# Kernel optimization log

Measured on AMD Instinct MI355X. Metric: run time of the kernel, lower is better.

Reference implementation:

```python
import jax, jax.numpy as jnp
import numpy as np

STRIDES = [8, 16, 32, 64, 128]
FSIZES = [64, 32, 16, 8, 4]          # 512x512 input
NUM_CLASSES = 80
POS_THR, NEG_THR = 0.5, 0.4          # MaxIOUAssigner thresholds
BETA = 1.0 / 9.0                      # SmoothL1 beta (from loss_bbox cfg)
BBOX_W = 10.0                         # SmoothL1 loss_weight
ALPHA, GAMMA = 0.25, 2.0              # sigmoid focal loss


def _gen_anchors():
    """RetinaNet-style grid anchors, xyxy, concatenated over levels -> [A,4]."""
    ratios = np.array([0.5, 1.0, 2.0])
    scales = 4.0 * 2.0 ** (np.arange(3) / 3.0)   # octave_base_scale=4, 3 octaves
    levels = []
    for s, f in zip(STRIDES, FSIZES):
        ws = (s * scales[None, :] / np.sqrt(ratios)[:, None]).reshape(-1)  # [9]
        hs = (s * scales[None, :] * np.sqrt(ratios)[:, None]).reshape(-1)
        c = (np.arange(f) + 0.5) * s
        sx, sy = np.meshgrid(c, c)
        cxy = np.stack([sx, sy], -1).reshape(-1, 1, 2)   # [f*f,1,2]
        wh = np.stack([ws, hs], -1)[None]                # [1,9,2]
        a = np.concatenate([cxy - wh / 2, cxy + wh / 2], -1).reshape(-1, 4)
        levels.append(a)
    return jnp.asarray(np.concatenate(levels, 0), dtype=jnp.float32)  # [49104,4]


def _iou(anchors, gt):  # [A,4],[M,4] -> [A,M]
    area_a = (anchors[:, 2] - anchors[:, 0]) * (anchors[:, 3] - anchors[:, 1])
    area_g = (gt[:, 2] - gt[:, 0]) * (gt[:, 3] - gt[:, 1])
    lt = jnp.maximum(anchors[:, None, :2], gt[None, :, :2])
    rb = jnp.minimum(anchors[:, None, 2:], gt[None, :, 2:])
    wh = jnp.clip(rb - lt, 0.0)
    inter = wh[..., 0] * wh[..., 1]
    return inter / jnp.maximum(area_a[:, None] + area_g[None, :] - inter, 1e-6)


def _encode(boxes, anchors):  # DeltaXYWH encode, target_stds = 1
    aw = anchors[:, 2] - anchors[:, 0]
    ah = anchors[:, 3] - anchors[:, 1]
    ax = (anchors[:, 0] + anchors[:, 2]) * 0.5
    ay = (anchors[:, 1] + anchors[:, 3]) * 0.5
    gw = jnp.maximum(boxes[:, 2] - boxes[:, 0], 1e-6)
    gh = jnp.maximum(boxes[:, 3] - boxes[:, 1], 1e-6)
    gx = (boxes[:, 0] + boxes[:, 2]) * 0.5
    gy = (boxes[:, 1] + boxes[:, 3]) * 0.5
    return jnp.stack([(gx - ax) / aw, (gy - ay) / ah,
                      jnp.log(gw / aw), jnp.log(gh / ah)], -1)


def _assign_one(gt_boxes, gt_labels, gt_mask, anchors):
    """Per-image: IoU match, pseudo-sample, gather matched GT, encode, masks."""
    iou = _iou(anchors, gt_boxes)                      # [A,M]
    iou = jnp.where(gt_mask[None, :], iou, -1.0)       # kill padded GTs
    best = jnp.argmax(iou, 1)                          # [A]
    best_iou = jnp.max(iou, 1)
    # matched index: >=0 matched, -1 background, -2 ignored
    idx = jnp.where(best_iou >= POS_THR, best,
                    jnp.where(best_iou < NEG_THR, -1, -2))
    pos = idx >= 0
    matched = jnp.where(pos[:, None], gt_boxes[best], 0.0)   # gather_based_on_match
    reg_t = _encode(matched, anchors)
    total = jnp.maximum(1.0, jnp.sum(pos.astype(jnp.float32)))
    mask_reg = pos.astype(jnp.float32)[:, None] / total      # [A,1] -> broadcast 4
    labels = jnp.where(pos, gt_labels[best], -1)             # bg/ignored -> -1
    mask_cls = (idx >= -1).astype(jnp.float32) / total       # matched + background
    return reg_t, mask_reg, labels, mask_cls


def setup_inputs() -> dict:
    key = jax.random.key(0)
    ks = jax.random.split(key, 6)
    B, M, A, C = 16, 100, 49104, NUM_CLASSES
    cls_score = jax.random.normal(ks[0], (B, A, C), jnp.float32)
    bbox_pred = jax.random.normal(ks[1], (B, A, 4), jnp.float32) * 0.1
    cxy = jax.random.uniform(ks[2], (B, M, 2), jnp.float32, 50.0, 462.0)
    wh = jax.random.uniform(ks[3], (B, M, 2), jnp.float32, 16.0, 128.0)
    target_boxes = jnp.concatenate([cxy - wh / 2, cxy + wh / 2], -1)
    target_labels = jax.random.randint(ks[4], (B, M), 0, C, jnp.int32)
    mask_labels = jax.random.randint(ks[5], (B, M), 0, 2, jnp.int32).astype(bool)
    return {"cls_score": cls_score, "bbox_pred": bbox_pred,
            "target_boxes": target_boxes, "target_labels": target_labels,
            "mask_labels": mask_labels}


def reference(cls_score, bbox_pred, target_boxes, target_labels, mask_labels):
    anchors = _gen_anchors()                                        # [A,4]
    reg_t, mask_reg, labels, mask_cls = jax.vmap(
        _assign_one, in_axes=(0, 0, 0, None))(
        target_boxes, target_labels, mask_labels, anchors)          # per image
    bs = float(cls_score.shape[0])
    # SmoothL1 (beta=1/9, weight 10), masked + normalized per image
    d = jnp.abs(bbox_pred - reg_t)
    l1 = jnp.where(d < BETA, 0.5 * d * d / BETA, d - 0.5 * BETA)
    loss_bbox = BBOX_W * jnp.sum(l1 * mask_reg) / bs
    # sigmoid focal loss
    t = jax.nn.one_hot(labels, NUM_CLASSES, dtype=cls_score.dtype)  # -1 -> all-zero
    bce = t * jax.nn.softplus(-cls_score) + (1.0 - t) * jax.nn.softplus(cls_score)
    p = jax.nn.sigmoid(cls_score)
    pt = t * p + (1.0 - t) * (1.0 - p)
    at = ALPHA * t + (1.0 - ALPHA) * (1.0 - t)
    focal = at * (1.0 - pt) ** GAMMA * bce
    loss_cls = jnp.sum(focal * mask_cls[..., None]) / bs
    return jnp.stack([loss_cls, loss_bbox])
```

## Files before the change

### kernel.cpp

```cpp
#include <hip/hip_runtime.h>

#define N_ANCH 49104
#define NB_IMG 16
#define NGT 100
#define NC 80
#define BPIA 128
#define BPIB 192
#define NA_BLK (BPIA * NB_IMG)
#define NB_BLK (BPIB * NB_IMG)
#define IMG_F4 (N_ANCH * NC / 4)
#define OFF_C NA_BLK
#define OFF_B (NA_BLK + NB_BLK)
#define OFF_P (NA_BLK + 2 * NB_BLK)

#define LOG2E 1.4426950408889634f
#define LN2   0.6931471805599453f
#define FSCALE (0.75f * LN2)

__device__ __forceinline__ float frcp(float x){ return __builtin_amdgcn_rcpf(x); }
__device__ __forceinline__ float fexp2(float x){ return __builtin_amdgcn_exp2f(x); }
__device__ __forceinline__ float flog2(float x){ return __builtin_amdgcn_logf(x); }

__device__ __forceinline__ float f0_acc(float x, float acc){
  float xl = x * LOG2E;
  float mx = fmaxf(xl, 0.f);
  float mn = fminf(xl, 0.f);
  float u  = fexp2(mn - mx);
  float w  = 1.0f + u;
  float lw = flog2(w);
  float g  = mn - lw;
  float p2 = fexp2(g + g);
  return fmaf(p2, lw + mx, acc);
}

__device__ __forceinline__ float corr_term(float x){
  float xl = x * LOG2E;
  float mx = fmaxf(xl, 0.f);
  float mn = fminf(xl, 0.f);
  float u  = fexp2(mn - mx);
  float w  = 1.0f + u;
  float lw = flog2(w);
  float p2   = fexp2(2.f * (mn - lw));
  float omp2 = fexp2(-2.f * (mx + lw));
  float sp   = LN2 * (lw + mx);
  float spn  = LN2 * (lw - mn);
  return 0.25f * omp2 * spn - 0.75f * p2 * sp;
}

__global__ __launch_bounds__(256, 6) void fused_loss_kernel(
    const float* __restrict__ cls,
    const float* __restrict__ bbox,
    const float* __restrict__ gtb,
    const int*   __restrict__ gtl,
    const unsigned char* __restrict__ gmask,
    float* __restrict__ ws)
{
  const int tid = threadIdx.x;
  const int wv = tid >> 6, ln = tid & 63;

  __shared__ float  s_r0[4], s_r1[4], s_r2[4];
  __shared__ float  s_wmin[4], s_wmax[4];
  __shared__ float4 s_cgt[NGT + 4];
  __shared__ float  s_carea[NGT + 4];
  __shared__ int    s_clab[NGT + 4];
  __shared__ int    s_cnt;

  const int idx = blockIdx.x;
  const int role = idx % 5;

  if (role < 2){
    int aid = (idx / 5) * 2 + role;
    int b = aid / BPIA, s = aid % BPIA;
    const float4* p = (const float4*)cls + (size_t)b * IMG_F4;
    float a0 = 0.f, a1 = 0.f, a2 = 0.f, a3 = 0.f;
    #pragma unroll 2
    for (int i = s * 256 + tid; i < IMG_F4; i += BPIA * 256){
      float4 c4 = p[i];
      a0 = f0_acc(c4.x, a0); a1 = f0_acc(c4.y, a1);
      a2 = f0_acc(c4.z, a2); a3 = f0_acc(c4.w, a3);
    }
    float acc = (a0 + a1) + (a2 + a3);
    #pragma unroll
    for (int o = 32; o > 0; o >>= 1) acc += __shfl_down(acc, o);
    if (ln == 0) s_r0[wv] = acc;
    __syncthreads();
    if (tid == 0) ws[aid] = s_r0[0] + s_r0[1] + s_r0[2] + s_r0[3];
    return;
  }

  int bid = (idx / 5) * 3 + (role - 2);
  int b = bid / BPIB, blkc = bid % BPIB;
  int a = blkc * 256 + tid;
  bool va = a < N_ANCH;

  float x1, y1, x2, y2, areaA;
  if (va){
    int f, lg, st, rel;
    if      (a < 36864){ f = 64; lg = 6; st = 8;   rel = a; }
    else if (a < 46080){ f = 32; lg = 5; st = 16;  rel = a - 36864; }
    else if (a < 48384){ f = 16; lg = 4; st = 32;  rel = a - 46080; }
    else if (a < 48960){ f = 8;  lg = 3; st = 64;  rel = a - 48384; }
    else               { f = 4;  lg = 2; st = 128; rel = a - 48960; }
    int cell = rel / 9;
    int k    = rel - cell * 9;
    int yy   = cell >> lg;
    int xx   = cell & (f - 1);
    int rr = (k >= 6) ? 2 : ((k >= 3) ? 1 : 0);
    int sc = k - rr * 3;
    double sq  = (rr == 0) ? 0.7071067811865476 : ((rr == 1) ? 1.0 : 1.4142135623730951);
    double scl = (sc == 0) ? 4.0 : ((sc == 1) ? 5.039684199579493 : 6.349604207872798);
    double ss  = (double)st * scl;
    double wd  = ss / sq, hd = ss * sq;
    double cxd = ((double)xx + 0.5) * (double)st;
    double cyd = ((double)yy + 0.5) * (double)st;
    x1 = (float)(cxd - wd * 0.5);
    y1 = (float)(cyd - hd * 0.5);
    x2 = (float)(cxd + wd * 0.5);
    y2 = (float)(cyd + hd * 0.5);
    areaA = (x2 - x1) * (y2 - y1);
  } else { x1 = 0.f; y1 = 3.0e38f; x2 = 0.f; y2 = -3.0e38f; areaA = 1.f; }

  {
    float wy1 = y1, wy2 = y2;
    #pragma unroll
    for (int o = 32; o > 0; o >>= 1){
      wy1 = fminf(wy1, __shfl_down(wy1, o));
      wy2 = fmaxf(wy2, __shfl_down(wy2, o));
    }
    if (ln == 0){ s_wmin[wv] = wy1; s_wmax[wv] = wy2; }
  }
  __syncthreads();

  if (wv == 0){
    const unsigned int* mw = (const unsigned int*)gmask;
    bool nf = false, ob = false;
    for (int i = ln; i < (NB_IMG * NGT) / 4; i += 64){
      unsigned int w = mw[i];
      nf |= (w != 0u && w != 0x3F800000u);
      ob |= ((w & 0xFFFFFF00u) != 0u);
    }
    bool byteLayout = __any((int)nf) && __any((int)ob);
    float ymin = fminf(fminf(s_wmin[0], s_wmin[1]), fminf(s_wmin[2], s_wmin[3]));
    float ymax = fmaxf(fmaxf(s_wmax[0], s_wmax[1]), fmaxf(s_wmax[2], s_wmax[3]));
    const float4* g4 = (const float4*)gtb;

    float4 g = g4[b * NGT + ln];
    int v = byteLayout ? (gmask[b * NGT + ln] != 0)
                       : (((const unsigned int*)gmask)[b * NGT + ln] != 0u);
    bool pass = v && (g.y < ymax) && (g.w > ymin);
    unsigned long long bal = __ballot(pass);
    int pre = __popcll(bal & ((1ull << ln) - 1ull));
    if (pass){
      s_cgt[pre] = g;
      s_carea[pre] = (g.z - g.x) * (g.w - g.y);
      s_clab[pre] = gtl[b * NGT + ln];
    }
    int c0 = __popcll(bal);
    bool pass1 = false; float4 g1;
    if (ln < NGT - 64){
      g1 = g4[b * NGT + 64 + ln];
      int v1 = byteLayout ? (gmask[b * NGT + 64 + ln] != 0)
                          : (((const unsigned int*)gmask)[b * NGT + 64 + ln] != 0u);
      pass1 = v1 && (g1.y < ymax) && (g1.w > ymin);
    }
    unsigned long long bal1 = __ballot(pass1);
    int pre1 = c0 + __popcll(bal1 & ((1ull << ln) - 1ull));
    if (pass1){
      s_cgt[pre1] = g1;
      s_carea[pre1] = (g1.z - g1.x) * (g1.w - g1.y);
      s_clab[pre1] = gtl[b * NGT + 64 + ln];
    }
    if (ln == 0){
      int cnt = c0 + __popcll(bal1);
      float4 far4; far4.x = 3e9f; far4.y = 3e9f; far4.z = 3e9f; far4.w = 3e9f;
      s_cgt[cnt] = far4;     s_carea[cnt] = 0.f;     s_clab[cnt] = 0;
      s_cgt[cnt + 1] = far4; s_carea[cnt + 1] = 0.f; s_clab[cnt + 1] = 0;
      s_cnt = (cnt + 1) & ~1;
    }
  }
  __syncthreads();

  float accC = 0.f, accB = 0.f, posf = 0.f;
  if (va){
    const int cntp = s_cnt;
    float best_iou = -1.f; int best = 0;
    for (int j = 0; j < cntp; j += 2){
      #pragma unroll
      for (int u2 = 0; u2 < 2; ++u2){
        int jj = j + u2;
        float4 g = s_cgt[jj];
        float lx = fmaxf(x1, g.x), ly = fmaxf(y1, g.y);
        float rx = fminf(x2, g.z), ry = fminf(y2, g.w);
        float iw = fmaxf(rx - lx, 0.f), ih = fmaxf(ry - ly, 0.f);
        float I  = iw * ih;
        float U  = (areaA + s_carea[jj]) - I;
        float iou = I * frcp(U);
        best = (iou > best_iou) ? jj : best;
        best_iou = fmaxf(iou, best_iou);
      }
    }
    bool pos = best_iou >= 0.5f;
    bool ign = (!pos) && (best_iou >= 0.4f);
    size_t row = (size_t)(b * N_ANCH + a) * NC;

    if (pos){
      posf = 1.f;
      float4 g = s_cgt[best];
      float aw = x2 - x1, ah = y2 - y1;
      float axc = (x1 + x2) * 0.5f, ayc = (y1 + y2) * 0.5f;
      float gw = fmaxf(g.z - g.x, 1e-6f), gh = fmaxf(g.w - g.y, 1e-6f);
      float gxc = (g.x + g.z) * 0.5f, gyc = (g.y + g.w) * 0.5f;
      float t0 = (gxc - axc) / aw, t1 = (gyc - ayc) / ah;
      float t2 = LN2 * flog2(gw * frcp(aw));
      float t3 = LN2 * flog2(gh * frcp(ah));
      float4 bp = ((const float4*)bbox)[(size_t)b * N_ANCH + a];
      const float BETA = 1.0f / 9.0f;
      float d0 = fabsf(bp.x - t0), d1 = fabsf(bp.y - t1);
      float d2 = fabsf(bp.z - t2), d3 = fabsf(bp.w - t3);
      accB += (d0 < BETA) ? 4.5f * d0 * d0 : d0 - 0.5f * BETA;
      accB += (d1 < BETA) ? 4.5f * d1 * d1 : d1 - 0.5f * BETA;
      accB += (d2 < BETA) ? 4.5f * d2 * d2 : d2 - 0.5f * BETA;
      accB += (d3 < BETA) ? 4.5f * d3 * d3 : d3 - 0.5f * BETA;
      accC += corr_term(cls[row + s_clab[best]]);
    }
    if (ign){
      const float4* cp = (const float4*)(cls + row);
      float i0 = 0.f, i1 = 0.f, i2 = 0.f, i3 = 0.f;
      #pragma unroll 4
      for (int v2 = 0; v2 < NC / 4; ++v2){
        float4 c4 = cp[v2];
        i0 = f0_acc(c4.x, i0); i1 = f0_acc(c4.y, i1);
        i2 = f0_acc(c4.z, i2); i3 = f0_acc(c4.w, i3);
      }
      accC -= FSCALE * ((i0 + i1) + (i2 + i3));
    }
  }

  #pragma unroll
  for (int o = 32; o > 0; o >>= 1){
    accC += __shfl_down(accC, o);
    accB += __shfl_down(accB, o);
    posf += __shfl_down(posf, o);
  }
  if (ln == 0){ s_r0[wv] = accC; s_r1[wv] = accB; s_r2[wv] = posf; }
  __syncthreads();
  if (tid == 0){
    ws[OFF_C + bid] = s_r0[0] + s_r0[1] + s_r0[2] + s_r0[3];
    ws[OFF_B + bid] = s_r1[0] + s_r1[1] + s_r1[2] + s_r1[3];
    ws[OFF_P + bid] = s_r2[0] + s_r2[1] + s_r2[2] + s_r2[3];
  }
}

__global__ void finalize_kernel(const float* __restrict__ ws,
                                float* __restrict__ out)
{
  __shared__ float sC[NB_IMG], sB[NB_IMG];
  const int tid = threadIdx.x;
  const int wv = tid >> 6, ln = tid & 63;
  #pragma unroll
  for (int i = 0; i < 2; ++i){
    int b = wv * 2 + i;
    float sa = 0.f;
    for (int k = ln; k < BPIA; k += 64) sa += ws[b * BPIA + k];
    float c = 0.f, bb = 0.f, p = 0.f;
    for (int k = ln; k < BPIB; k += 64){
      c  += ws[OFF_C + b * BPIB + k];
      bb += ws[OFF_B + b * BPIB + k];
      p  += ws[OFF_P + b * BPIB + k];
    }
    c += FSCALE * sa;
    #pragma unroll
    for (int o = 32; o > 0; o >>= 1){
      c += __shfl_down(c, o); bb += __shfl_down(bb, o); p += __shfl_down(p, o);
    }
    if (ln == 0){
      float tot = fmaxf(p, 1.f);
      sC[b] = c / tot;
      sB[b] = bb / tot;
    }
  }
  __syncthreads();
  if (tid == 0){
    float lc = 0.f, lb = 0.f;
    #pragma unroll
    for (int b = 0; b < NB_IMG; ++b){ lc += sC[b]; lb += sB[b]; }
    out[0] = lc / 16.f;
    out[1] = 10.f * lb / 16.f;
  }
}

extern "C" void kernel_launch(void* const* d_in, const int* in_sizes, int n_in,
                              void* d_out, int out_size, void* d_ws, size_t ws_size,
                              hipStream_t stream) {
  const float* cls  = (const float*)d_in[0];
  const float* bbox = (const float*)d_in[1];
  const float* gtb  = (const float*)d_in[2];
  const int*   gtl  = (const int*)d_in[3];
  const unsigned char* gmask = (const unsigned char*)d_in[4];

  float* ws = (float*)d_ws;

  int total_blocks = (NA_BLK + NB_BLK) / 5 * 5;
  fused_loss_kernel<<<total_blocks, 256, 0, stream>>>(cls, bbox, gtb, gtl, gmask, ws);
  finalize_kernel<<<1, 512, 0, stream>>>(ws, (float*)d_out);
}
```

Before: 65.42 us.

## Fuse dense focal pass into per-tile assignment blocks with shared-memory weights

The separate dense-sweep blocks over all class logits and the per-anchor re-read of ignored rows are replaced by one schedule. Each block assigns 512 anchors, stores a per-anchor weight and label in shared memory, then streams that tile's contiguous logits with coalesced float4 loads. Ignored anchors are masked by weight instead of subtracted afterwards, and the positive-label correction is picked from the streamed data. This removes the duplicate reads for ignored rows and the scattered gather, but it serialises assignment before streaming inside each block and adds an integer divide per float4.

New measurement: 57.25 us. 12.5% less time.

```diff
diff --git a/kernel.cpp b/kernel.cpp
--- a/kernel.cpp
+++ b/kernel.cpp
@@ -4,14 +4,11 @@
 #define NB_IMG 16
 #define NGT 100
 #define NC 80
-#define BPIA 128
-#define BPIB 192
-#define NA_BLK (BPIA * NB_IMG)
-#define NB_BLK (BPIB * NB_IMG)
-#define IMG_F4 (N_ANCH * NC / 4)
-#define OFF_C NA_BLK
-#define OFF_B (NA_BLK + NB_BLK)
-#define OFF_P (NA_BLK + 2 * NB_BLK)
+#define BPI 96
+#define APB 512
+#define NBLK (BPI * NB_IMG)
+#define OFF_B NBLK
+#define OFF_P (2 * NBLK)
 
 #define LOG2E 1.4426950408889634f
 #define LN2   0.6931471805599453f
@@ -21,7 +18,7 @@
 __device__ __forceinline__ float fexp2(float x){ return __builtin_amdgcn_exp2f(x); }
 __device__ __forceinline__ float flog2(float x){ return __builtin_amdgcn_logf(x); }
 
-__device__ __forceinline__ float f0_acc(float x, float acc){
+__device__ __forceinline__ float f0_term(float x){
   float xl = x * LOG2E;
   float mx = fmaxf(xl, 0.f);
   float mn = fminf(xl, 0.f);
@@ -29,8 +26,7 @@
   float w  = 1.0f + u;
   float lw = flog2(w);
   float g  = mn - lw;
-  float p2 = fexp2(g + g);
-  return fmaf(p2, lw + mx, acc);
+  return fexp2(g + g) * (lw + mx);
 }
 
 __device__ __forceinline__ float corr_term(float x){
@@ -57,71 +53,55 @@
 {
   const int tid = threadIdx.x;
   const int wv = tid >> 6, ln = tid & 63;
-
-  __shared__ float  s_r0[4], s_r1[4], s_r2[4];
-  __shared__ float  s_wmin[4], s_wmax[4];
+  const int b  = blockIdx.y;
+  const int a0 = blockIdx.x * APB;
+  const int bid = b * BPI + blockIdx.x;
+
   __shared__ float4 s_cgt[NGT + 4];
   __shared__ float  s_carea[NGT + 4];
   __shared__ int    s_clab[NGT + 4];
+  __shared__ float  s_w[APB];
+  __shared__ int    s_lab[APB];
+  __shared__ float  s_wmin[4], s_wmax[4];
+  __shared__ float  s_r0[4], s_r1[4], s_r2[4];
   __shared__ int    s_cnt;
 
-  const int idx = blockIdx.x;
-  const int role = idx % 5;
-
-  if (role < 2){
-    int aid = (idx / 5) * 2 + role;
-    int b = aid / BPIA, s = aid % BPIA;
-    const float4* p = (const float4*)cls + (size_t)b * IMG_F4;
-    float a0 = 0.f, a1 = 0.f, a2 = 0.f, a3 = 0.f;
-    #pragma unroll 2
-    for (int i = s * 256 + tid; i < IMG_F4; i += BPIA * 256){
-      float4 c4 = p[i];
-      a0 = f0_acc(c4.x, a0); a1 = f0_acc(c4.y, a1);
-      a2 = f0_acc(c4.z, a2); a3 = f0_acc(c4.w, a3);
-    }
-    float acc = (a0 + a1) + (a2 + a3);
-    #pragma unroll
-    for (int o = 32; o > 0; o >>= 1) acc += __shfl_down(acc, o);
-    if (ln == 0) s_r0[wv] = acc;
-    __syncthreads();
-    if (tid == 0) ws[aid] = s_r0[0] + s_r0[1] + s_r0[2] + s_r0[3];
-    return;
-  }
-
-  int bid = (idx / 5) * 3 + (role - 2);
-  int b = bid / BPIB, blkc = bid % BPIB;
-  int a = blkc * 256 + tid;
-  bool va = a < N_ANCH;
-
-  float x1, y1, x2, y2, areaA;
-  if (va){
-    int f, lg, st, rel;
-    if      (a < 36864){ f = 64; lg = 6; st = 8;   rel = a; }
-    else if (a < 46080){ f = 32; lg = 5; st = 16;  rel = a - 36864; }
-    else if (a < 48384){ f = 16; lg = 4; st = 32;  rel = a - 46080; }
-    else if (a < 48960){ f = 8;  lg = 3; st = 64;  rel = a - 48384; }
-    else               { f = 4;  lg = 2; st = 128; rel = a - 48960; }
-    int cell = rel / 9;
-    int k    = rel - cell * 9;
-    int yy   = cell >> lg;
-    int xx   = cell & (f - 1);
-    int rr = (k >= 6) ? 2 : ((k >= 3) ? 1 : 0);
-    int sc = k - rr * 3;
-    double sq  = (rr == 0) ? 0.7071067811865476 : ((rr == 1) ? 1.0 : 1.4142135623730951);
-    double scl = (sc == 0) ? 4.0 : ((sc == 1) ? 5.039684199579493 : 6.349604207872798);
-    double ss  = (double)st * scl;
-    double wd  = ss / sq, hd = ss * sq;
-    double cxd = ((double)xx + 0.5) * (double)st;
-    double cyd = ((double)yy + 0.5) * (double)st;
-    x1 = (float)(cxd - wd * 0.5);
-    y1 = (float)(cyd - hd * 0.5);
-    x2 = (float)(cxd + wd * 0.5);
-    y2 = (float)(cyd + hd * 0.5);
-    areaA = (x2 - x1) * (y2 - y1);
-  } else { x1 = 0.f; y1 = 3.0e38f; x2 = 0.f; y2 = -3.0e38f; areaA = 1.f; }
+  float ax1[2], ay1[2], ax2[2], ay2[2], aarea[2];
+  #pragma unroll
+  for (int r = 0; r < 2; ++r){
+    int a = a0 + r * 256 + tid;
+    if (a < N_ANCH){
+      int f, lg, st, rel;
+      if      (a < 36864){ f = 64; lg = 6; st = 8;   rel = a; }
+      else if (a < 46080){ f = 32; lg = 5; st = 16;  rel = a - 36864; }
+      else if (a < 48384){ f = 16; lg = 4; st = 32;  rel = a - 46080; }
+      else if (a < 48960){ f = 8;  lg = 3; st = 64;  rel = a - 48384; }
+      else               { f = 4;  lg = 2; st = 128; rel = a - 48960; }
+      int cell = rel / 9;
+      int k    = rel - cell * 9;
+      int yy   = cell >> lg;
+      int xx   = cell & (f - 1);
+      int rr = (k >= 6) ? 2 : ((k >= 3) ? 1 : 0);
+      int sc = k - rr * 3;
+      double sq  = (rr == 0) ? 0.7071067811865476 : ((rr == 1) ? 1.0 : 1.4142135623730951);
+      double scl = (sc == 0) ? 4.0 : ((sc == 1) ? 5.039684199579493 : 6.349604207872798);
+      double ss  = (double)st * scl;
+      double wd  = ss / sq, hd = ss * sq;
+      double cxd = ((double)xx + 0.5) * (double)st;
+      double cyd = ((double)yy + 0.5) * (double)st;
+      ax1[r] = (float)(cxd - wd * 0.5);
+      ay1[r] = (float)(cyd - hd * 0.5);
+      ax2[r] = (float)(cxd + wd * 0.5);
+      ay2[r] = (float)(cyd + hd * 0.5);
+      aarea[r] = (ax2[r] - ax1[r]) * (ay2[r] - ay1[r]);
+    } else {
+      ax1[r] = 0.f; ay1[r] = 3.0e38f; ax2[r] = 0.f; ay2[r] = -3.0e38f; aarea[r] = 1.f;
+    }
+  }
 
   {
-    float wy1 = y1, wy2 = y2;
+    float wy1 = fminf(ay1[0], ay1[1]);
+    float wy2 = fmaxf(ay2[0], ay2[1]);
     #pragma unroll
     for (int o = 32; o > 0; o >>= 1){
       wy1 = fminf(wy1, __shfl_down(wy1, o));
@@ -180,9 +160,13 @@
   }
   __syncthreads();
 
-  float accC = 0.f, accB = 0.f, posf = 0.f;
-  if (va){
-    const int cntp = s_cnt;
+  float accB = 0.f, posf = 0.f, fcorr = 0.f;
+  const int cntp = s_cnt;
+  #pragma unroll
+  for (int r = 0; r < 2; ++r){
+    int row = r * 256 + tid;
+    int a = a0 + row;
+    float x1 = ax1[r], y1 = ay1[r], x2 = ax2[r], y2 = ay2[r], areaA = aarea[r];
     float best_iou = -1.f; int best = 0;
     for (int j = 0; j < cntp; j += 2){
       #pragma unroll
@@ -199,12 +183,14 @@
         best_iou = fmaxf(iou, best_iou);
       }
     }
-    bool pos = best_iou >= 0.5f;
-    bool ign = (!pos) && (best_iou >= 0.4f);
-    size_t row = (size_t)(b * N_ANCH + a) * NC;
+    bool va  = a < N_ANCH;
+    bool pos = va && (best_iou >= 0.5f);
+    bool ign = va && !pos && (best_iou >= 0.4f);
+    s_w[row]   = (va && !ign) ? 1.f : 0.f;
+    s_lab[row] = pos ? s_clab[best] : -1;
 
     if (pos){
-      posf = 1.f;
+      posf += 1.f;
       float4 g = s_cgt[best];
       float aw = x2 - x1, ah = y2 - y1;
       float axc = (x1 + x2) * 0.5f, ayc = (y1 + y2) * 0.5f;
@@ -221,20 +207,28 @@
       accB += (d1 < BETA) ? 4.5f * d1 * d1 : d1 - 0.5f * BETA;
       accB += (d2 < BETA) ? 4.5f * d2 * d2 : d2 - 0.5f * BETA;
       accB += (d3 < BETA) ? 4.5f * d3 * d3 : d3 - 0.5f * BETA;
-      accC += corr_term(cls[row + s_clab[best]]);
-    }
-    if (ign){
-      const float4* cp = (const float4*)(cls + row);
-      float i0 = 0.f, i1 = 0.f, i2 = 0.f, i3 = 0.f;
-      #pragma unroll 4
-      for (int v2 = 0; v2 < NC / 4; ++v2){
-        float4 c4 = cp[v2];
-        i0 = f0_acc(c4.x, i0); i1 = f0_acc(c4.y, i1);
-        i2 = f0_acc(c4.z, i2); i3 = f0_acc(c4.w, i3);
-      }
-      accC -= FSCALE * ((i0 + i1) + (i2 + i3));
-    }
-  }
+    }
+  }
+  __syncthreads();
+
+  const int nvalid = min(N_ANCH - a0, APB);
+  const int nf4 = nvalid * 20;
+  const float4* cp = (const float4*)(cls + (size_t)(b * N_ANCH + a0) * NC);
+  float fraw = 0.f;
+  for (int i = tid; i < nf4; i += 256){
+    float4 c4 = cp[i];
+    int row = i / 20;
+    int cb  = (i - row * 20) * 4;
+    float s = (f0_term(c4.x) + f0_term(c4.y)) + (f0_term(c4.z) + f0_term(c4.w));
+    fraw = fmaf(s_w[row], s, fraw);
+    int lab = s_lab[row];
+    if ((unsigned)(lab - cb) < 4u){
+      int o = lab - cb;
+      float xe = (o == 0) ? c4.x : (o == 1) ? c4.y : (o == 2) ? c4.z : c4.w;
+      fcorr += corr_term(xe);
+    }
+  }
+  float accC = fmaf(FSCALE, fraw, fcorr);
 
   #pragma unroll
   for (int o = 32; o > 0; o >>= 1){
@@ -245,7 +239,7 @@
   if (ln == 0){ s_r0[wv] = accC; s_r1[wv] = accB; s_r2[wv] = posf; }
   __syncthreads();
   if (tid == 0){
-    ws[OFF_C + bid] = s_r0[0] + s_r0[1] + s_r0[2] + s_r0[3];
+    ws[bid]         = s_r0[0] + s_r0[1] + s_r0[2] + s_r0[3];
     ws[OFF_B + bid] = s_r1[0] + s_r1[1] + s_r1[2] + s_r1[3];
     ws[OFF_P + bid] = s_r2[0] + s_r2[1] + s_r2[2] + s_r2[3];
   }
@@ -260,15 +254,12 @@
   #pragma unroll
   for (int i = 0; i < 2; ++i){
     int b = wv * 2 + i;
-    float sa = 0.f;
-    for (int k = ln; k < BPIA; k += 64) sa += ws[b * BPIA + k];
     float c = 0.f, bb = 0.f, p = 0.f;
-    for (int k = ln; k < BPIB; k += 64){
-      c  += ws[OFF_C + b * BPIB + k];
-      bb += ws[OFF_B + b * BPIB + k];
-      p  += ws[OFF_P + b * BPIB + k];
-    }
-    c += FSCALE * sa;
+    for (int k = ln; k < BPI; k += 64){
+      c  += ws[b * BPI + k];
+      bb += ws[OFF_B + b * BPI + k];
+      p  += ws[OFF_P + b * BPI + k];
+    }
     #pragma unroll
     for (int o = 32; o > 0; o >>= 1){
       c += __shfl_down(c, o); bb += __shfl_down(bb, o); p += __shfl_down(p, o);
@@ -300,7 +291,7 @@
 
   float* ws = (float*)d_ws;
 
-  int total_blocks = (NA_BLK + NB_BLK) / 5 * 5;
-  fused_loss_kernel<<<total_blocks, 256, 0, stream>>>(cls, bbox, gtb, gtl, gmask, ws);
+  dim3 grid(BPI, NB_IMG);
+  fused_loss_kernel<<<grid, 256, 0, stream>>>(cls, bbox, gtb, gtl, gmask, ws);
   finalize_kernel<<<1, 512, 0, stream>>>(ws, (float*)d_out);
 }
```
